# Optimization experiments

Hardware: AMD Instinct MI355X
Metric: run time of the kernel (lower is better)

Reference implementation:

```python
import jax, jax.numpy as jnp
import numpy as np

ALPHA = 0.2  # LeakyReLU negative slope


def setup_inputs() -> dict:
    key = jax.random.key(0)
    k1, k2, k3, k4 = jax.random.split(key, 4)
    N, Fin, Fout = 8192, 256, 64
    inputs = {
        "input": jax.random.normal(k1, (N, Fin), dtype=jnp.float32),
        "adj": jax.random.randint(k2, (N, N), 0, 2, dtype=jnp.int32),
        "W": jax.random.normal(k3, (Fin, Fout), dtype=jnp.float32) * (1.414 * np.sqrt(2.0 / (Fin + Fout))),
        "a": jax.random.normal(k4, (2 * Fout, 1), dtype=jnp.float32) * (1.414 * np.sqrt(2.0 / (2 * Fout + 1))),
    }
    return inputs


def reference(input, adj, W, a):
    # h: [N, Fout]
    h = input @ W
    Fout = h.shape[1]
    # Decompose pairwise score: e[i,j] = leakyrelu(h[i]@a1 + h[j]@a2)
    # (mathematically identical to the original concat+matmul construction,
    #  but avoids the O(N^2 * 2F) intermediate)
    a1, a2 = a[:Fout, 0], a[Fout:, 0]
    s1 = h @ a1  # [N]
    s2 = h @ a2  # [N]
    e = jax.nn.leaky_relu(s1[:, None] + s2[None, :], negative_slope=ALPHA)  # [N, N]
    # Mask non-edges with -10 (as in the original), row softmax
    masked = jnp.where(adj > 0, e, jnp.float32(-10.0))
    attention = jax.nn.softmax(masked, axis=1)
    # dropout p=0.0 (eval/reference mode): identity
    h_prime = attention @ h  # [N, Fout]
    return jax.nn.elu(h_prime)  # concat=True path
```

## Files before the change

kernel.cpp:

```cpp
#include <hip/hip_runtime.h>
#include <hip/hip_bf16.h>
#include <cstdint>
#include <cstddef>

#define NN 8192
#define FIN 256
#define FOUT 64
#define ALPHA_SLOPE 0.2f
#define EXP_M10 4.5399929762484854e-05f

#define JSPLIT 8
#define STRIP 64
#define NSTRIP ((NN / JSPLIT) / STRIP)
#define RB 128
#define WPITCH 144
#define HPITCH 144
#define CP 68

typedef short s16x8 __attribute__((ext_vector_type(8)));
typedef float f32x4 __attribute__((ext_vector_type(4)));
typedef int   i32x4 __attribute__((ext_vector_type(4)));

__device__ __forceinline__ unsigned short f2bf(float x) {
    union { float f; uint32_t u; } v; v.f = x;
    uint32_t u = v.u;
    return (unsigned short)((u + 0x7FFFu + ((u >> 16) & 1u)) >> 16);
}

__device__ __forceinline__ unsigned int pk2(float lo, float hi) {
    return (unsigned int)f2bf(lo) | ((unsigned int)f2bf(hi) << 16);
}

__device__ __forceinline__ uint2 wpack4(i32x4 a, float4 v, float s1v) {
    float x0 = s1v + v.x, x1 = s1v + v.y, x2 = s1v + v.z, x3 = s1v + v.w;
    float w0 = (a.x > 0) ? __expf(fmaxf(x0, ALPHA_SLOPE * x0)) : EXP_M10;
    float w1 = (a.y > 0) ? __expf(fmaxf(x1, ALPHA_SLOPE * x1)) : EXP_M10;
    float w2 = (a.z > 0) ? __expf(fmaxf(x2, ALPHA_SLOPE * x2)) : EXP_M10;
    float w3 = (a.w > 0) ? __expf(fmaxf(x3, ALPHA_SLOPE * x3)) : EXP_M10;
    uint2 r; r.x = pk2(w0, w1); r.y = pk2(w2, w3);
    return r;
}

__global__ __launch_bounds__(256) void k_h(
    const float* __restrict__ input, const float* __restrict__ W,
    const float* __restrict__ a,
    unsigned short* __restrict__ htg, float* __restrict__ s1, float* __restrict__ s2)
{
    __shared__ __align__(16) unsigned short tile[64][28];
    const int wid  = threadIdx.x >> 6;
    const int lane = threadIdx.x & 63;
    const int i0   = blockIdx.x * 16;
    const int r0   = wid * 4;
    const float* inb = input + (size_t)(i0 + r0) * FIN;

    float acc0 = 0.f, acc1 = 0.f, acc2 = 0.f, acc3 = 0.f;
    #pragma unroll 4
    for (int c = 0; c < FIN; c += 4) {
        float w0 = W[(c + 0) * FOUT + lane];
        float w1 = W[(c + 1) * FOUT + lane];
        float w2 = W[(c + 2) * FOUT + lane];
        float w3 = W[(c + 3) * FOUT + lane];
        float4 x0 = *(const float4*)(inb + 0 * FIN + c);
        float4 x1 = *(const float4*)(inb + 1 * FIN + c);
        float4 x2 = *(const float4*)(inb + 2 * FIN + c);
        float4 x3 = *(const float4*)(inb + 3 * FIN + c);
        acc0 = fmaf(x0.x, w0, fmaf(x0.y, w1, fmaf(x0.z, w2, fmaf(x0.w, w3, acc0))));
        acc1 = fmaf(x1.x, w0, fmaf(x1.y, w1, fmaf(x1.z, w2, fmaf(x1.w, w3, acc1))));
        acc2 = fmaf(x2.x, w0, fmaf(x2.y, w1, fmaf(x2.z, w2, fmaf(x2.w, w3, acc2))));
        acc3 = fmaf(x3.x, w0, fmaf(x3.y, w1, fmaf(x3.z, w2, fmaf(x3.w, w3, acc3))));
    }

    const float a1v = a[lane], a2v = a[FOUT + lane];
    float accs[4] = {acc0, acc1, acc2, acc3};
    #pragma unroll
    for (int r = 0; r < 4; ++r) {
        float v1 = accs[r] * a1v;
        float v2 = accs[r] * a2v;
        #pragma unroll
        for (int off = 32; off; off >>= 1) {
            v1 += __shfl_xor(v1, off);
            v2 += __shfl_xor(v2, off);
        }
        if (lane == 0) { s1[i0 + r0 + r] = v1; s2[i0 + r0 + r] = v2; }
        tile[lane][r0 + r] = f2bf(accs[r]);
    }
    __syncthreads();

    const int feat = threadIdx.x >> 2;
    const int cg   = (threadIdx.x & 3) * 4;
    uint2 q = *(const uint2*)&tile[feat][cg];
    *(uint2*)(htg + (size_t)feat * NN + i0 + cg) = q;
}

__global__ __launch_bounds__(512, 4) void k_attn(
    const int* __restrict__ adj,
    const unsigned short* __restrict__ htg,
    const float* __restrict__ s1g, const float* __restrict__ s2g,
    float* __restrict__ slabs)
{
    __shared__ __align__(16) unsigned char wbuf[2][RB * WPITCH];
    __shared__ __align__(16) unsigned char hbuf[2][64 * HPITCH];

    const int t    = threadIdx.x;
    const int wid  = t >> 6;
    const int lane = t & 63;
    const int bi   = blockIdx.x >> 3;
    const int js   = blockIdx.x & 7;
    const int i0   = bi * RB;
    const int jbase = js * (NN / JSPLIT);
    const int m    = lane & 15;
    const int quad = lane >> 4;

    const int srow  = t >> 2;
    const int scol  = (t & 3) * 16;
    const int sfeat = t >> 3;
    const int scol2 = (t & 7) * 8;
    const float s1v = s1g[i0 + srow];

    const short bd = (m == 0) ? (short)0x3F80 : (short)0;
    const s16x8 bden = {bd, bd, bd, bd, bd, bd, bd, bd};

    f32x4 acc0 = {0,0,0,0}, acc1 = {0,0,0,0}, acc2 = {0,0,0,0},
          acc3 = {0,0,0,0}, accD = {0,0,0,0};

    const int* adjrow = adj + (size_t)(i0 + srow) * NN + jbase;
    const unsigned short* hrow = htg + (size_t)sfeat * NN + jbase;

    {
        i32x4  a0 = *(const i32x4*)(adjrow + scol);
        i32x4  a1 = *(const i32x4*)(adjrow + scol + 4);
        i32x4  a2 = *(const i32x4*)(adjrow + scol + 8);
        i32x4  a3 = *(const i32x4*)(adjrow + scol + 12);
        float4 v0 = *(const float4*)(s2g + jbase + scol);
        float4 v1 = *(const float4*)(s2g + jbase + scol + 4);
        float4 v2 = *(const float4*)(s2g + jbase + scol + 8);
        float4 v3 = *(const float4*)(s2g + jbase + scol + 12);
        s16x8  h0 = *(const s16x8*)(hrow + scol2);

        uint2 pA = wpack4(a0, v0, s1v), pB = wpack4(a1, v1, s1v);
        uint2 pC = wpack4(a2, v2, s1v), pD = wpack4(a3, v3, s1v);
        uint4 q0 = {pA.x, pA.y, pB.x, pB.y};
        uint4 q1 = {pC.x, pC.y, pD.x, pD.y};
        unsigned char* wd = &wbuf[0][srow * WPITCH + (t & 3) * 32];
        *(uint4*)(wd)      = q0;
        *(uint4*)(wd + 16) = q1;
        *(s16x8*)&hbuf[0][sfeat * HPITCH + scol2 * 2] = h0;
    }
    __syncthreads();

    for (int s = 0; s < NSTRIP; ++s) {
        const int cur = s & 1, nxt = cur ^ 1;
        const bool more = (s + 1 < NSTRIP);

        i32x4 a0, a1, a2, a3; float4 v0, v1, v2, v3; s16x8 h0;
        if (more) {
            const int jn = (s + 1) * STRIP;
            a0 = *(const i32x4*)(adjrow + jn + scol);
            a1 = *(const i32x4*)(adjrow + jn + scol + 4);
            a2 = *(const i32x4*)(adjrow + jn + scol + 8);
            a3 = *(const i32x4*)(adjrow + jn + scol + 12);
            v0 = *(const float4*)(s2g + jbase + jn + scol);
            v1 = *(const float4*)(s2g + jbase + jn + scol + 4);
            v2 = *(const float4*)(s2g + jbase + jn + scol + 8);
            v3 = *(const float4*)(s2g + jbase + jn + scol + 12);
            h0 = *(const s16x8*)(hrow + jn + scol2);
        }

        #pragma unroll
        for (int kk = 0; kk < 2; ++kk) {
            const int cb = kk * 64 + quad * 16;
            s16x8 af = *(const s16x8*)&wbuf[cur][(wid * 16 + m) * WPITCH + cb];
            s16x8 b0 = *(const s16x8*)&hbuf[cur][(m +  0) * HPITCH + cb];
            s16x8 b1 = *(const s16x8*)&hbuf[cur][(m + 16) * HPITCH + cb];
            s16x8 b2 = *(const s16x8*)&hbuf[cur][(m + 32) * HPITCH + cb];
            s16x8 b3 = *(const s16x8*)&hbuf[cur][(m + 48) * HPITCH + cb];
            acc0 = __builtin_amdgcn_mfma_f32_16x16x32_bf16(af, b0,   acc0, 0, 0, 0);
            acc1 = __builtin_amdgcn_mfma_f32_16x16x32_bf16(af, b1,   acc1, 0, 0, 0);
            acc2 = __builtin_amdgcn_mfma_f32_16x16x32_bf16(af, b2,   acc2, 0, 0, 0);
            acc3 = __builtin_amdgcn_mfma_f32_16x16x32_bf16(af, b3,   acc3, 0, 0, 0);
            accD = __builtin_amdgcn_mfma_f32_16x16x32_bf16(af, bden, accD, 0, 0, 0);
        }

        if (more) {
            uint2 pA = wpack4(a0, v0, s1v), pB = wpack4(a1, v1, s1v);
            uint2 pC = wpack4(a2, v2, s1v), pD = wpack4(a3, v3, s1v);
            uint4 q0 = {pA.x, pA.y, pB.x, pB.y};
            uint4 q1 = {pC.x, pC.y, pD.x, pD.y};
            unsigned char* wd = &wbuf[nxt][srow * WPITCH + (t & 3) * 32];
            *(uint4*)(wd)      = q0;
            *(uint4*)(wd + 16) = q1;
            *(s16x8*)&hbuf[nxt][sfeat * HPITCH + scol2 * 2] = h0;
        }
        __syncthreads();
    }

    float* slab = slabs + (size_t)js * ((size_t)NN * CP);
    const int r0 = i0 + wid * 16 + quad * 4;
    #pragma unroll
    for (int reg = 0; reg < 4; ++reg) {
        size_t ro = (size_t)(r0 + reg) * CP;
        slab[ro +  0 + m] = acc0[reg];
        slab[ro + 16 + m] = acc1[reg];
        slab[ro + 32 + m] = acc2[reg];
        slab[ro + 48 + m] = acc3[reg];
        if (m == 0) slab[ro + 64] = accD[reg];
    }
}

__global__ __launch_bounds__(256) void k_norm(
    const float* __restrict__ slabs, float* __restrict__ out)
{
    int gid = blockIdx.x * 256 + threadIdx.x;
    int i = gid >> 6, k = gid & 63;
    float num = 0.f, den = 0.f;
    #pragma unroll
    for (int js = 0; js < JSPLIT; ++js) {
        const float* row = slabs + (size_t)js * ((size_t)NN * CP) + (size_t)i * CP;
        num += row[k];
        den += row[64];
    }
    float v = num / den;
    out[gid] = (v > 0.f) ? v : (__expf(v) - 1.f);
}

extern "C" void kernel_launch(void* const* d_in, const int* in_sizes, int n_in,
                              void* d_out, int out_size, void* d_ws, size_t ws_size,
                              hipStream_t stream) {
    const float* input = (const float*)d_in[0];
    const int*   adj   = (const int*)d_in[1];
    const float* W     = (const float*)d_in[2];
    const float* a     = (const float*)d_in[3];
    float* out = (float*)d_out;

    char* ws = (char*)d_ws;
    float* slabs = (float*)ws;
    size_t off = (size_t)JSPLIT * NN * CP * sizeof(float);
    unsigned short* htg = (unsigned short*)(ws + off);
    off += (size_t)FOUT * NN * sizeof(unsigned short);
    float* s1 = (float*)(ws + off); off += NN * sizeof(float);
    float* s2 = (float*)(ws + off);

    k_h   <<<NN / 16, 256, 0, stream>>>(input, W, a, htg, s1, s2);
    k_attn<<<(NN / RB) * JSPLIT, 512, 0, stream>>>(adj, htg, s1, s2, slabs);
    k_norm<<<NN * FOUT / 256, 256, 0, stream>>>(slabs, out);
}
```

Baseline: 421.9 us.

## Halve attention row block, split features across waves, compute denominator on VALU

The row block shrinks from 128 to 64 rows. The 8 waves are rearranged as 4 row groups by 2 feature halves, so each wave issues 2 MFMAs per k-step instead of 5. The extra MFMA against a ones vector that produced the softmax denominator is removed. The denominator is now summed in registers from the bf16-rounded weights and reduced with shuffles, and launch bounds ask for 8 blocks per CU to raise occupancy. In exchange, twice as many blocks each reload h and s2, so reads of those arrays roughly double, and each thread now packs 8 weights per strip instead of 16.

```diff
diff --git a/kernel.cpp b/kernel.cpp
--- a/kernel.cpp
+++ b/kernel.cpp
@@ -12,7 +12,7 @@
 #define JSPLIT 8
 #define STRIP 64
 #define NSTRIP ((NN / JSPLIT) / STRIP)
-#define RB 128
+#define RB 64
 #define WPITCH 144
 #define HPITCH 144
 #define CP 68
@@ -27,18 +27,18 @@
     return (unsigned short)((u + 0x7FFFu + ((u >> 16) & 1u)) >> 16);
 }
 
-__device__ __forceinline__ unsigned int pk2(float lo, float hi) {
-    return (unsigned int)f2bf(lo) | ((unsigned int)f2bf(hi) << 16);
-}
-
-__device__ __forceinline__ uint2 wpack4(i32x4 a, float4 v, float s1v) {
-    float x0 = s1v + v.x, x1 = s1v + v.y, x2 = s1v + v.z, x3 = s1v + v.w;
-    float w0 = (a.x > 0) ? __expf(fmaxf(x0, ALPHA_SLOPE * x0)) : EXP_M10;
-    float w1 = (a.y > 0) ? __expf(fmaxf(x1, ALPHA_SLOPE * x1)) : EXP_M10;
-    float w2 = (a.z > 0) ? __expf(fmaxf(x2, ALPHA_SLOPE * x2)) : EXP_M10;
-    float w3 = (a.w > 0) ? __expf(fmaxf(x3, ALPHA_SLOPE * x3)) : EXP_M10;
-    uint2 r; r.x = pk2(w0, w1); r.y = pk2(w2, w3);
-    return r;
+__device__ __forceinline__ unsigned int rpack2(float a, float b, float& dsum) {
+    union { float f; uint32_t u; } va, vb, ra, rb;
+    va.f = a; vb.f = b;
+    ra.u = (va.u + 0x7FFFu + ((va.u >> 16) & 1u)) & 0xFFFF0000u;
+    rb.u = (vb.u + 0x7FFFu + ((vb.u >> 16) & 1u)) & 0xFFFF0000u;
+    dsum += ra.f + rb.f;
+    return (ra.u >> 16) | rb.u;
+}
+
+__device__ __forceinline__ float wval(int a, float s2v, float s1v) {
+    float x = s1v + s2v;
+    return (a > 0) ? __expf(fmaxf(x, ALPHA_SLOPE * x)) : EXP_M10;
 }
 
 __global__ __launch_bounds__(256) void k_h(
@@ -92,7 +92,7 @@
     *(uint2*)(htg + (size_t)feat * NN + i0 + cg) = q;
 }
 
-__global__ __launch_bounds__(512, 4) void k_attn(
+__global__ __launch_bounds__(512, 8) void k_attn(
     const int* __restrict__ adj,
     const unsigned short* __restrict__ htg,
     const float* __restrict__ s1g, const float* __restrict__ s2g,
@@ -110,41 +110,33 @@
     const int jbase = js * (NN / JSPLIT);
     const int m    = lane & 15;
     const int quad = lane >> 4;
-
-    const int srow  = t >> 2;
-    const int scol  = (t & 3) * 16;
-    const int sfeat = t >> 3;
-    const int scol2 = (t & 7) * 8;
+    const int rg   = wid >> 1;
+    const int fg   = wid & 1;
+
+    const int srow = t >> 3;
+    const int scol = (t & 7) * 8;
     const float s1v = s1g[i0 + srow];
 
-    const short bd = (m == 0) ? (short)0x3F80 : (short)0;
-    const s16x8 bden = {bd, bd, bd, bd, bd, bd, bd, bd};
-
-    f32x4 acc0 = {0,0,0,0}, acc1 = {0,0,0,0}, acc2 = {0,0,0,0},
-          acc3 = {0,0,0,0}, accD = {0,0,0,0};
+    f32x4 acc0 = {0,0,0,0}, acc1 = {0,0,0,0};
+    float dsum = 0.f;
 
     const int* adjrow = adj + (size_t)(i0 + srow) * NN + jbase;
-    const unsigned short* hrow = htg + (size_t)sfeat * NN + jbase;
+    const unsigned short* hrow = htg + (size_t)srow * NN + jbase;
+    const float* s2p = s2g + jbase;
 
     {
         i32x4  a0 = *(const i32x4*)(adjrow + scol);
         i32x4  a1 = *(const i32x4*)(adjrow + scol + 4);
-        i32x4  a2 = *(const i32x4*)(adjrow + scol + 8);
-        i32x4  a3 = *(const i32x4*)(adjrow + scol + 12);
-        float4 v0 = *(const float4*)(s2g + jbase + scol);
-        float4 v1 = *(const float4*)(s2g + jbase + scol + 4);
-        float4 v2 = *(const float4*)(s2g + jbase + scol + 8);
-        float4 v3 = *(const float4*)(s2g + jbase + scol + 12);
-        s16x8  h0 = *(const s16x8*)(hrow + scol2);
-
-        uint2 pA = wpack4(a0, v0, s1v), pB = wpack4(a1, v1, s1v);
-        uint2 pC = wpack4(a2, v2, s1v), pD = wpack4(a3, v3, s1v);
-        uint4 q0 = {pA.x, pA.y, pB.x, pB.y};
-        uint4 q1 = {pC.x, pC.y, pD.x, pD.y};
-        unsigned char* wd = &wbuf[0][srow * WPITCH + (t & 3) * 32];
-        *(uint4*)(wd)      = q0;
-        *(uint4*)(wd + 16) = q1;
-        *(s16x8*)&hbuf[0][sfeat * HPITCH + scol2 * 2] = h0;
+        float4 v0 = *(const float4*)(s2p + scol);
+        float4 v1 = *(const float4*)(s2p + scol + 4);
+        s16x8  h0 = *(const s16x8*)(hrow + scol);
+        uint4 q;
+        q.x = rpack2(wval(a0.x, v0.x, s1v), wval(a0.y, v0.y, s1v), dsum);
+        q.y = rpack2(wval(a0.z, v0.z, s1v), wval(a0.w, v0.w, s1v), dsum);
+        q.z = rpack2(wval(a1.x, v1.x, s1v), wval(a1.y, v1.y, s1v), dsum);
+        q.w = rpack2(wval(a1.z, v1.z, s1v), wval(a1.w, v1.w, s1v), dsum);
+        *(uint4*)&wbuf[0][srow * WPITCH + (t & 7) * 16] = q;
+        *(s16x8*)&hbuf[0][srow * HPITCH + (t & 7) * 16] = h0;
     }
     __syncthreads();
 
@@ -152,59 +144,50 @@
         const int cur = s & 1, nxt = cur ^ 1;
         const bool more = (s + 1 < NSTRIP);
 
-        i32x4 a0, a1, a2, a3; float4 v0, v1, v2, v3; s16x8 h0;
+        i32x4 a0, a1; float4 v0, v1; s16x8 h0;
         if (more) {
             const int jn = (s + 1) * STRIP;
             a0 = *(const i32x4*)(adjrow + jn + scol);
             a1 = *(const i32x4*)(adjrow + jn + scol + 4);
-            a2 = *(const i32x4*)(adjrow + jn + scol + 8);
-            a3 = *(const i32x4*)(adjrow + jn + scol + 12);
-            v0 = *(const float4*)(s2g + jbase + jn + scol);
-            v1 = *(const float4*)(s2g + jbase + jn + scol + 4);
-            v2 = *(const float4*)(s2g + jbase + jn + scol + 8);
-            v3 = *(const float4*)(s2g + jbase + jn + scol + 12);
-            h0 = *(const s16x8*)(hrow + jn + scol2);
+            v0 = *(const float4*)(s2p + jn + scol);
+            v1 = *(const float4*)(s2p + jn + scol + 4);
+            h0 = *(const s16x8*)(hrow + jn + scol);
         }
 
         #pragma unroll
         for (int kk = 0; kk < 2; ++kk) {
             const int cb = kk * 64 + quad * 16;
-            s16x8 af = *(const s16x8*)&wbuf[cur][(wid * 16 + m) * WPITCH + cb];
-            s16x8 b0 = *(const s16x8*)&hbuf[cur][(m +  0) * HPITCH + cb];
-            s16x8 b1 = *(const s16x8*)&hbuf[cur][(m + 16) * HPITCH + cb];
-            s16x8 b2 = *(const s16x8*)&hbuf[cur][(m + 32) * HPITCH + cb];
-            s16x8 b3 = *(const s16x8*)&hbuf[cur][(m + 48) * HPITCH + cb];
-            acc0 = __builtin_amdgcn_mfma_f32_16x16x32_bf16(af, b0,   acc0, 0, 0, 0);
-            acc1 = __builtin_amdgcn_mfma_f32_16x16x32_bf16(af, b1,   acc1, 0, 0, 0);
-            acc2 = __builtin_amdgcn_mfma_f32_16x16x32_bf16(af, b2,   acc2, 0, 0, 0);
-            acc3 = __builtin_amdgcn_mfma_f32_16x16x32_bf16(af, b3,   acc3, 0, 0, 0);
-            accD = __builtin_amdgcn_mfma_f32_16x16x32_bf16(af, bden, accD, 0, 0, 0);
+            s16x8 af = *(const s16x8*)&wbuf[cur][(rg * 16 + m) * WPITCH + cb];
+            s16x8 b0 = *(const s16x8*)&hbuf[cur][(fg * 32 + m) * HPITCH + cb];
+            s16x8 b1 = *(const s16x8*)&hbuf[cur][(fg * 32 + 16 + m) * HPITCH + cb];
+            acc0 = __builtin_amdgcn_mfma_f32_16x16x32_bf16(af, b0, acc0, 0, 0, 0);
+            acc1 = __builtin_amdgcn_mfma_f32_16x16x32_bf16(af, b1, acc1, 0, 0, 0);
         }
 
         if (more) {
-            uint2 pA = wpack4(a0, v0, s1v), pB = wpack4(a1, v1, s1v);
-            uint2 pC = wpack4(a2, v2, s1v), pD = wpack4(a3, v3, s1v);
-            uint4 q0 = {pA.x, pA.y, pB.x, pB.y};
-            uint4 q1 = {pC.x, pC.y, pD.x, pD.y};
-            unsigned char* wd = &wbuf[nxt][srow * WPITCH + (t & 3) * 32];
-            *(uint4*)(wd)      = q0;
-            *(uint4*)(wd + 16) = q1;
-            *(s16x8*)&hbuf[nxt][sfeat * HPITCH + scol2 * 2] = h0;
+            uint4 q;
+            q.x = rpack2(wval(a0.x, v0.x, s1v), wval(a0.y, v0.y, s1v), dsum);
+            q.y = rpack2(wval(a0.z, v0.z, s1v), wval(a0.w, v0.w, s1v), dsum);
+            q.z = rpack2(wval(a1.x, v1.x, s1v), wval(a1.y, v1.y, s1v), dsum);
+            q.w = rpack2(wval(a1.z, v1.z, s1v), wval(a1.w, v1.w, s1v), dsum);
+            *(uint4*)&wbuf[nxt][srow * WPITCH + (t & 7) * 16] = q;
+            *(s16x8*)&hbuf[nxt][srow * HPITCH + (t & 7) * 16] = h0;
         }
         __syncthreads();
     }
 
     float* slab = slabs + (size_t)js * ((size_t)NN * CP);
-    const int r0 = i0 + wid * 16 + quad * 4;
+    const int r0 = i0 + rg * 16 + quad * 4;
     #pragma unroll
     for (int reg = 0; reg < 4; ++reg) {
         size_t ro = (size_t)(r0 + reg) * CP;
-        slab[ro +  0 + m] = acc0[reg];
-        slab[ro + 16 + m] = acc1[reg];
-        slab[ro + 32 + m] = acc2[reg];
-        slab[ro + 48 + m] = acc3[reg];
-        if (m == 0) slab[ro + 64] = accD[reg];
-    }
+        slab[ro + fg * 32 + m]      = acc0[reg];
+        slab[ro + fg * 32 + 16 + m] = acc1[reg];
+    }
+    dsum += __shfl_xor(dsum, 1);
+    dsum += __shfl_xor(dsum, 2);
+    dsum += __shfl_xor(dsum, 4);
+    if ((t & 7) == 0) slab[(size_t)(i0 + srow) * CP + 64] = dsum;
 }
 
 __global__ __launch_bounds__(256) void k_norm(
```

After: 413.3 us. 2.0% less time.
